# Kernel optimization log

Hardware: AMD Instinct MI355X
Metric: run time of the kernel (lower is better)

## Reference

```python
import jax, jax.numpy as jnp
import numpy as np

N = 4096
IN_F = 512
OUT_F = 64
N_HEADS = 8
ALPHA = 0.2
NEG_INF = -9e15


def setup_inputs() -> dict:
    key = jax.random.key(0)
    k1, k2, k3, k4 = jax.random.split(key, 4)
    h = jax.random.normal(k1, (N, IN_F), dtype=jnp.float32)
    adj = jax.random.randint(k2, (N, N), 0, 2, dtype=jnp.int32)
    W = jax.random.normal(k3, (IN_F, OUT_F * N_HEADS), dtype=jnp.float32) * (1.414 / np.sqrt(IN_F))
    a = jax.random.normal(k4, (2 * OUT_F, 1), dtype=jnp.float32) * 0.1
    return {"h": h, "adj": adj, "W": W, "a": a}


def reference(h, adj, W, a):
    # Wh: [N, H, F]
    Wh = (h @ W).reshape(N, N_HEADS, OUT_F)
    # The all-pairs concat + matmul with a ([2F,1], shared across heads)
    # decomposes exactly: e[i,j,h] = leakyrelu(Wh[i,h]@a[:F] + Wh[j,h]@a[F:])
    a_src = a[:OUT_F, 0]
    a_dst = a[OUT_F:, 0]
    src = jnp.einsum('nhf,f->nh', Wh, a_src)  # [N, H]
    dst = jnp.einsum('nhf,f->nh', Wh, a_dst)  # [N, H]
    e = src[:, None, :] + dst[None, :, :]      # [N, N, H]
    e = jnp.where(e > 0, e, ALPHA * e)         # leaky relu
    e = jnp.where(adj[:, :, None] > 0, e, NEG_INF)
    attention = jax.nn.softmax(e, axis=1)      # softmax over neighbors j
    h_prime = jnp.einsum('ijh,jhf->ihf', attention, Wh)  # [N, H, F]
    out = h_prime.reshape(N, N_HEADS * OUT_F)
    return jax.nn.elu(out)
```

## Files before the change

### kernel.cpp

```cpp
#include <hip/hip_runtime.h>
#include <hip/hip_bf16.h>


typedef unsigned short ushort_t;
typedef __attribute__((ext_vector_type(8))) short bf16x8;
typedef __attribute__((ext_vector_type(4))) float f32x4;

#define LOG2E 1.4426950408889634f

__device__ __forceinline__ ushort_t f2bf(float x) {
    unsigned u = __builtin_bit_cast(unsigned, x);
    u += 0x7FFFu + ((u >> 16) & 1u);
    return (ushort_t)(u >> 16);
}

__global__ __launch_bounds__(256) void transpose_w(const float* __restrict__ W,
                                                   ushort_t* __restrict__ WT) {
    __shared__ ushort_t t[32][33];
    int bx = blockIdx.x & 15, by = blockIdx.x >> 4;
    int tx = threadIdx.x & 31, ty = threadIdx.x >> 5;
#pragma unroll
    for (int i = 0; i < 32; i += 8)
        t[ty + i][tx] = f2bf(W[(by * 32 + ty + i) * 512 + bx * 32 + tx]);
    __syncthreads();
#pragma unroll
    for (int i = 0; i < 32; i += 8)
        WT[(bx * 32 + ty + i) * 512 + by * 32 + tx] = t[tx][ty + i];
}

__global__ __launch_bounds__(256, 4) void gemm_pack(const ushort_t* __restrict__ WT,
                                                    const float* __restrict__ h,
                                                    const float* __restrict__ a,
                                                    ushort_t* __restrict__ WhT,
                                                    float* __restrict__ expA,
                                                    float* __restrict__ expC,
                                                    float* __restrict__ expB,
                                                    float* __restrict__ expD,
                                                    const int* __restrict__ adj,
                                                    unsigned char* __restrict__ pk) {
    __shared__ __align__(16) ushort_t Al[2][64][72];
    __shared__ __align__(16) ushort_t Bl[2][64][72];
    __shared__ float asrc[64], adst[64];
    __shared__ float sred[2][4][64];
    int tid = threadIdx.x;
    if (blockIdx.x >= 512) {
        int pbid = blockIdx.x - 512;
        int wv = tid >> 6, lane = tid & 63;
        int row = pbid * 4 + wv;
        const int* ap = adj + (unsigned)row * 4096 + lane;
        unsigned char* pp = pk + (unsigned)row * 512;
        int g = lane;
        int sv = ((g >> 2) & 1) * 4 + (g & 3);
        int cpar = g >> 3;
#pragma unroll 2
        for (int t = 0; t < 8; t++) {
            unsigned long long m[8];
#pragma unroll
            for (int c8 = 0; c8 < 8; c8++)
                m[c8] = __ballot(ap[(t * 8 + c8) * 64] > 0);
            if (lane < 16) {
                unsigned w = 0;
#pragma unroll
                for (int kq = 0; kq < 4; kq++) {
                    unsigned b = (unsigned)(m[2 * kq + cpar] >> (8 * sv)) & 0xFFu;
                    w |= b << (8 * kq);
                }
                *(unsigned*)(pp + g * 32 + t * 4) = w;
            }
        }
        return;
    }
    int wave = tid >> 6, lane = tid & 63, quad = lane >> 4, nn = lane & 15;
    int mb = blockIdx.x & 7, nb = blockIdx.x >> 3;
    if (tid < 64) {
        asrc[tid] = a[tid] * LOG2E;
        adst[tid] = a[64 + tid] * LOG2E;
    }
    int r = tid >> 2, s0 = tid & 3;
    const ushort_t* Ag = WT + (unsigned)((mb * 64 + r) * 512 + s0 * 8);
    const float* Bg = h + (unsigned)((nb * 64 + r) * 512 + s0 * 8);
    bf16x8 pA0 = *(const bf16x8*)(Ag);
    bf16x8 pA1 = *(const bf16x8*)(Ag + 32);
    float4 pb0 = *(const float4*)(Bg);
    float4 pb1 = *(const float4*)(Bg + 4);
    float4 pb2 = *(const float4*)(Bg + 32);
    float4 pb3 = *(const float4*)(Bg + 36);
    f32x4 acc[4] = {};
#pragma unroll 2
    for (int t = 0; t < 8; t++) {
        int cb = t & 1;
        *(bf16x8*)&Al[cb][r][s0 * 8] = pA0;
        *(bf16x8*)&Al[cb][r][s0 * 8 + 32] = pA1;
        bf16x8 bv;
        bv[0] = (short)f2bf(pb0.x); bv[1] = (short)f2bf(pb0.y);
        bv[2] = (short)f2bf(pb0.z); bv[3] = (short)f2bf(pb0.w);
        bv[4] = (short)f2bf(pb1.x); bv[5] = (short)f2bf(pb1.y);
        bv[6] = (short)f2bf(pb1.z); bv[7] = (short)f2bf(pb1.w);
        *(bf16x8*)&Bl[cb][r][s0 * 8] = bv;
        bv[0] = (short)f2bf(pb2.x); bv[1] = (short)f2bf(pb2.y);
        bv[2] = (short)f2bf(pb2.z); bv[3] = (short)f2bf(pb2.w);
        bv[4] = (short)f2bf(pb3.x); bv[5] = (short)f2bf(pb3.y);
        bv[6] = (short)f2bf(pb3.z); bv[7] = (short)f2bf(pb3.w);
        *(bf16x8*)&Bl[cb][r][s0 * 8 + 32] = bv;
        if (t < 7) {
            int ko = (t + 1) * 64;
            pA0 = *(const bf16x8*)(Ag + ko);
            pA1 = *(const bf16x8*)(Ag + ko + 32);
            pb0 = *(const float4*)(Bg + ko);
            pb1 = *(const float4*)(Bg + ko + 4);
            pb2 = *(const float4*)(Bg + ko + 32);
            pb3 = *(const float4*)(Bg + ko + 36);
        }
        if (t > 0) {
            int pb = cb ^ 1;
            bf16x8 af0 = *(const bf16x8*)&Al[pb][wave * 16 + nn][quad * 8];
            bf16x8 af1 = *(const bf16x8*)&Al[pb][wave * 16 + nn][32 + quad * 8];
#pragma unroll
            for (int nt = 0; nt < 4; nt++) {
                bf16x8 b0 = *(const bf16x8*)&Bl[pb][nt * 16 + nn][quad * 8];
                bf16x8 b1 = *(const bf16x8*)&Bl[pb][nt * 16 + nn][32 + quad * 8];
                acc[nt] = __builtin_amdgcn_mfma_f32_16x16x32_bf16(af0, b0, acc[nt], 0, 0, 0);
                acc[nt] = __builtin_amdgcn_mfma_f32_16x16x32_bf16(af1, b1, acc[nt], 0, 0, 0);
            }
        }
        __syncthreads();
    }
    {
        bf16x8 af0 = *(const bf16x8*)&Al[1][wave * 16 + nn][quad * 8];
        bf16x8 af1 = *(const bf16x8*)&Al[1][wave * 16 + nn][32 + quad * 8];
#pragma unroll
        for (int nt = 0; nt < 4; nt++) {
            bf16x8 b0 = *(const bf16x8*)&Bl[1][nt * 16 + nn][quad * 8];
            bf16x8 b1 = *(const bf16x8*)&Bl[1][nt * 16 + nn][32 + quad * 8];
            acc[nt] = __builtin_amdgcn_mfma_f32_16x16x32_bf16(af0, b0, acc[nt], 0, 0, 0);
            acc[nt] = __builtin_amdgcn_mfma_f32_16x16x32_bf16(af1, b1, acc[nt], 0, 0, 0);
        }
    }
    int row0 = mb * 64 + wave * 16 + quad * 4;
    int col0 = nb * 64 + nn;
    int f0i = wave * 16 + quad * 4;
#pragma unroll
    for (int nt = 0; nt < 4; nt++) {
        float s = 0.f, d = 0.f;
#pragma unroll
        for (int rr = 0; rr < 4; rr++) {
            float v = acc[nt][rr];
            WhT[(unsigned)((row0 + rr) * 4096 + col0 + nt * 16)] = f2bf(v);
            s += v * asrc[f0i + rr];
            d += v * adst[f0i + rr];
        }
        s += __shfl_xor(s, 16); s += __shfl_xor(s, 32);
        d += __shfl_xor(d, 16); d += __shfl_xor(d, 32);
        if (quad == 0) { sred[0][wave][nt * 16 + nn] = s; sred[1][wave][nt * 16 + nn] = d; }
    }
    __syncthreads();
    if (tid < 64) {
        float s = sred[0][0][tid] + sred[0][1][tid] + sred[0][2][tid] + sred[0][3][tid];
        unsigned idx = mb * 4096 + nb * 64 + tid;
        expA[idx] = __builtin_amdgcn_exp2f(s);
        expC[idx] = __builtin_amdgcn_exp2f(0.2f * s);
    } else if (tid < 128) {
        int c = tid - 64;
        float d = sred[1][0][c] + sred[1][1][c] + sred[1][2][c] + sred[1][3][c];
        unsigned idx = mb * 4096 + nb * 64 + c;
        expB[idx] = __builtin_amdgcn_exp2f(d);
        expD[idx] = __builtin_amdgcn_exp2f(0.2f * d);
    }
}

__global__ __launch_bounds__(512, 4) void gat_attn(const unsigned char* __restrict__ pk,
                                                   const ushort_t* __restrict__ WhT,
                                                   const float* __restrict__ expA,
                                                   const float* __restrict__ expC,
                                                   const float* __restrict__ expB,
                                                   const float* __restrict__ expD,
                                                   float* __restrict__ out) {
    __shared__ __align__(16) ushort_t Vb[2][128][136];
    __shared__ float denomp[4][2][32];
    int tid = threadIdx.x;
    int wave = tid >> 6, lane = tid & 63, quad = lane >> 4, nn = lane & 15;
    int hb = blockIdx.x >> 7, ib = blockIdx.x & 127;
    int i0 = ib * 32;
    int whead = wave & 1, jq = wave >> 1;
    int g = jq * 4 + quad;
    int head = hb * 2 + whead;
    float Ai0 = expA[head * 4096 + i0 + nn];
    float Ci0 = expC[head * 4096 + i0 + nn];
    float Ai1 = expA[head * 4096 + i0 + 16 + nn];
    float Ci1 = expC[head * 4096 + i0 + 16 + nn];
    const unsigned char* mpA = pk + (unsigned)(i0 + nn) * 512 + g * 32;
    const unsigned char* mpB = mpA + 16 * 512;
    const float* Bp = expB + (unsigned)head * 4096 + jq * 32 + quad * 8;
    const float* Dp = expD + (unsigned)head * 4096 + jq * 32 + quad * 8;
    int vrow = tid >> 2, vs = tid & 3;
    const ushort_t* Vg = WhT + (unsigned)(hb * 128 + vrow) * 4096 + vs * 8;
    bf16x8 onef;
#pragma unroll
    for (int i = 0; i < 8; i++) onef[i] = (short)0x3F80;
    f32x4 acc[2][4] = {};
    f32x4 accd[2] = {};
    bf16x8 pv[4];
    float4 pBD[4];
    pv[0] = *(const bf16x8*)(Vg);
    pv[1] = *(const bf16x8*)(Vg + 32);
    pv[2] = *(const bf16x8*)(Vg + 64);
    pv[3] = *(const bf16x8*)(Vg + 96);
    pBD[0] = *(const float4*)(Bp);
    pBD[1] = *(const float4*)(Bp + 4);
    pBD[2] = *(const float4*)(Dp);
    pBD[3] = *(const float4*)(Dp + 4);
    unsigned mcA = *(const unsigned*)(mpA);
    unsigned mcB = *(const unsigned*)(mpB);
    unsigned mnA = 0, mnB = 0;
    for (int t = 0; t < 8; t++) {
#pragma unroll
        for (int u = 0; u < 4; u++) {
            int kb = t * 4 + u;
            int cb = kb & 1;
            *(bf16x8*)&Vb[cb][vrow][vs * 8] = pv[0];
            *(bf16x8*)&Vb[cb][vrow][vs * 8 + 32] = pv[1];
            *(bf16x8*)&Vb[cb][vrow][vs * 8 + 64] = pv[2];
            *(bf16x8*)&Vb[cb][vrow][vs * 8 + 96] = pv[3];
            float4 Bv0 = pBD[0], Bv1 = pBD[1], Dv0 = pBD[2], Dv1 = pBD[3];
            bf16x8 af0, af1;
            {
                unsigned w0, w1, w2, w3, w4, w5, w6, w7;
                float w;
                w = fmaxf(Ai0 * Bv0.x, Ci0 * Dv0.x);
                w0 = __builtin_bit_cast(unsigned, w) & 0xFFFF0000u;
                w0 &= (unsigned)__builtin_amdgcn_sbfe(mcA, u * 8 + 0, 1);
                w = fmaxf(Ai0 * Bv0.y, Ci0 * Dv0.y);
                w1 = __builtin_bit_cast(unsigned, w) & 0xFFFF0000u;
                w1 &= (unsigned)__builtin_amdgcn_sbfe(mcA, u * 8 + 1, 1);
                w = fmaxf(Ai0 * Bv0.z, Ci0 * Dv0.z);
                w2 = __builtin_bit_cast(unsigned, w) & 0xFFFF0000u;
                w2 &= (unsigned)__builtin_amdgcn_sbfe(mcA, u * 8 + 2, 1);
                w = fmaxf(Ai0 * Bv0.w, Ci0 * Dv0.w);
                w3 = __builtin_bit_cast(unsigned, w) & 0xFFFF0000u;
                w3 &= (unsigned)__builtin_amdgcn_sbfe(mcA, u * 8 + 3, 1);
                w = fmaxf(Ai0 * Bv1.x, Ci0 * Dv1.x);
                w4 = __builtin_bit_cast(unsigned, w) & 0xFFFF0000u;
                w4 &= (unsigned)__builtin_amdgcn_sbfe(mcA, u * 8 + 4, 1);
                w = fmaxf(Ai0 * Bv1.y, Ci0 * Dv1.y);
                w5 = __builtin_bit_cast(unsigned, w) & 0xFFFF0000u;
                w5 &= (unsigned)__builtin_amdgcn_sbfe(mcA, u * 8 + 5, 1);
                w = fmaxf(Ai0 * Bv1.z, Ci0 * Dv1.z);
                w6 = __builtin_bit_cast(unsigned, w) & 0xFFFF0000u;
                w6 &= (unsigned)__builtin_amdgcn_sbfe(mcA, u * 8 + 6, 1);
                w = fmaxf(Ai0 * Bv1.w, Ci0 * Dv1.w);
                w7 = __builtin_bit_cast(unsigned, w) & 0xFFFF0000u;
                w7 &= (unsigned)__builtin_amdgcn_sbfe(mcA, u * 8 + 7, 1);
                uint4 pq;
                pq.x = __builtin_amdgcn_perm(w1, w0, 0x07060302u);
                pq.y = __builtin_amdgcn_perm(w3, w2, 0x07060302u);
                pq.z = __builtin_amdgcn_perm(w5, w4, 0x07060302u);
                pq.w = __builtin_amdgcn_perm(w7, w6, 0x07060302u);
                af0 = __builtin_bit_cast(bf16x8, pq);
                w = fmaxf(Ai1 * Bv0.x, Ci1 * Dv0.x);
                w0 = __builtin_bit_cast(unsigned, w) & 0xFFFF0000u;
                w0 &= (unsigned)__builtin_amdgcn_sbfe(mcB, u * 8 + 0, 1);
                w = fmaxf(Ai1 * Bv0.y, Ci1 * Dv0.y);
                w1 = __builtin_bit_cast(unsigned, w) & 0xFFFF0000u;
                w1 &= (unsigned)__builtin_amdgcn_sbfe(mcB, u * 8 + 1, 1);
                w = fmaxf(Ai1 * Bv0.z, Ci1 * Dv0.z);
                w2 = __builtin_bit_cast(unsigned, w) & 0xFFFF0000u;
                w2 &= (unsigned)__builtin_amdgcn_sbfe(mcB, u * 8 + 2, 1);
                w = fmaxf(Ai1 * Bv0.w, Ci1 * Dv0.w);
                w3 = __builtin_bit_cast(unsigned, w) & 0xFFFF0000u;
                w3 &= (unsigned)__builtin_amdgcn_sbfe(mcB, u * 8 + 3, 1);
                w = fmaxf(Ai1 * Bv1.x, Ci1 * Dv1.x);
                w4 = __builtin_bit_cast(unsigned, w) & 0xFFFF0000u;
                w4 &= (unsigned)__builtin_amdgcn_sbfe(mcB, u * 8 + 4, 1);
                w = fmaxf(Ai1 * Bv1.y, Ci1 * Dv1.y);
                w5 = __builtin_bit_cast(unsigned, w) & 0xFFFF0000u;
                w5 &= (unsigned)__builtin_amdgcn_sbfe(mcB, u * 8 + 5, 1);
                w = fmaxf(Ai1 * Bv1.z, Ci1 * Dv1.z);
                w6 = __builtin_bit_cast(unsigned, w) & 0xFFFF0000u;
                w6 &= (unsigned)__builtin_amdgcn_sbfe(mcB, u * 8 + 6, 1);
                w = fmaxf(Ai1 * Bv1.w, Ci1 * Dv1.w);
                w7 = __builtin_bit_cast(unsigned, w) & 0xFFFF0000u;
                w7 &= (unsigned)__builtin_amdgcn_sbfe(mcB, u * 8 + 7, 1);
                pq.x = __builtin_amdgcn_perm(w1, w0, 0x07060302u);
                pq.y = __builtin_amdgcn_perm(w3, w2, 0x07060302u);
                pq.z = __builtin_amdgcn_perm(w5, w4, 0x07060302u);
                pq.w = __builtin_amdgcn_perm(w7, w6, 0x07060302u);
                af1 = __builtin_bit_cast(bf16x8, pq);
            }
            if (u == 3) { mcA = mnA; mcB = mnB; }
            __syncthreads();
            __builtin_amdgcn_sched_barrier(0);
            if (kb < 31) {
                const ushort_t* vp = Vg + (kb + 1) * 128;
                pv[0] = *(const bf16x8*)(vp);
                pv[1] = *(const bf16x8*)(vp + 32);
                pv[2] = *(const bf16x8*)(vp + 64);
                pv[3] = *(const bf16x8*)(vp + 96);
                pBD[0] = *(const float4*)(Bp + (kb + 1) * 128);
                pBD[1] = *(const float4*)(Bp + (kb + 1) * 128 + 4);
                pBD[2] = *(const float4*)(Dp + (kb + 1) * 128);
                pBD[3] = *(const float4*)(Dp + (kb + 1) * 128 + 4);
            }
            if (u == 0 && t < 7) {
                mnA = *(const unsigned*)(mpA + (t + 1) * 4);
                mnB = *(const unsigned*)(mpB + (t + 1) * 4);
            }
#pragma unroll
            for (int nt = 0; nt < 4; nt++) {
                bf16x8 bv = *(const bf16x8*)&Vb[cb][whead * 64 + nt * 16 + nn][jq * 32 + quad * 8];
                acc[0][nt] = __builtin_amdgcn_mfma_f32_16x16x32_bf16(af0, bv, acc[0][nt], 0, 0, 0);
                acc[1][nt] = __builtin_amdgcn_mfma_f32_16x16x32_bf16(af1, bv, acc[1][nt], 0, 0, 0);
            }
            accd[0] = __builtin_amdgcn_mfma_f32_16x16x32_bf16(af0, onef, accd[0], 0, 0, 0);
            accd[1] = __builtin_amdgcn_mfma_f32_16x16x32_bf16(af1, onef, accd[1], 0, 0, 0);
        }
    }
    __syncthreads();
    if (nn == 0) {
#pragma unroll
        for (int s = 0; s < 2; s++)
#pragma unroll
            for (int rr = 0; rr < 4; rr++)
                denomp[jq][whead][s * 16 + quad * 4 + rr] = accd[s][rr];
    }
    float (*cmb)[3][64][32] = reinterpret_cast<float (*)[3][64][32]>(&Vb[0][0][0]);
    if (jq > 0) {
#pragma unroll
        for (int s = 0; s < 2; s++)
#pragma unroll
            for (int nt = 0; nt < 4; nt++)
                *(f32x4*)&cmb[whead][jq - 1][lane][s * 16 + nt * 4] = acc[s][nt];
    }
    __syncthreads();
    if (jq == 0) {
#pragma unroll
        for (int s = 0; s < 2; s++) {
#pragma unroll
            for (int nt = 0; nt < 4; nt++) {
                f32x4 o = acc[s][nt]
                        + *(const f32x4*)&cmb[whead][0][lane][s * 16 + nt * 4]
                        + *(const f32x4*)&cmb[whead][1][lane][s * 16 + nt * 4]
                        + *(const f32x4*)&cmb[whead][2][lane][s * 16 + nt * 4];
#pragma unroll
                for (int rr = 0; rr < 4; rr++) {
                    int il = s * 16 + quad * 4 + rr;
                    float dnm = fmaxf(denomp[0][whead][il] + denomp[1][whead][il]
                                    + denomp[2][whead][il] + denomp[3][whead][il], 1e-30f);
                    float v = o[rr] / dnm;
                    v = v > 0.f ? v : __expf(v) - 1.f;
                    out[(unsigned)(i0 + il) * 512 + hb * 128 + whead * 64 + nt * 16 + nn] = v;
                }
            }
        }
    }
}

extern "C" void kernel_launch(void* const* d_in, const int* in_sizes, int n_in,
                              void* d_out, int out_size, void* d_ws, size_t ws_size,
                              hipStream_t stream) {
    const float* h   = (const float*)d_in[0];
    const int*   adj = (const int*)d_in[1];
    const float* W   = (const float*)d_in[2];
    const float* a   = (const float*)d_in[3];

    char* ws = (char*)d_ws;
    ushort_t* WhT = (ushort_t*)ws;
    ushort_t* WT  = (ushort_t*)(ws + (4u << 20));
    float* expA = (float*)(ws + (4u << 20) + (512u << 10));
    float* expC = expA + 8 * 4096;
    float* expB = expC + 8 * 4096;
    float* expD = expB + 8 * 4096;
    unsigned char* pkm = (unsigned char*)(ws + (5u << 20));

    transpose_w<<<256, 256, 0, stream>>>(W, WT);
    gemm_pack<<<1536, 256, 0, stream>>>(WT, h, a, WhT, expA, expC, expB, expD,
                                        adj, pkm);
    gat_attn<<<512, 512, 0, stream>>>(pkm, WhT, expA, expC, expB, expD,
                                      (float*)d_out);
}
```

Before: 169.7 us.

## Load V fragments directly from global into registers, drop LDS staging and barriers

The attention loop no longer stages the WhT tile through double-buffered shared memory. Each lane now loads its MFMA B-operand fragments straight from global memory into ping-pong register sets, which removes the per-iteration LDS stores, LDS reads and __syncthreads. The MFMA block is also wrapped in s_setprio to favour matrix issue. In exchange, each V element is fetched from global or L2 by several waves, since the two heads share rows and the reads are strided, and register pressure rises with two fragment sets.

```diff
diff --git a/kernel.cpp b/kernel.cpp
--- a/kernel.cpp
+++ b/kernel.cpp
@@ -168,6 +168,79 @@
     }
 }
 
+__device__ __forceinline__ bf16x8 gen_frag(float Ai, float Ci,
+                                           float4 Bv0, float4 Bv1,
+                                           float4 Dv0, float4 Dv1,
+                                           unsigned mc, int u) {
+    unsigned w0, w1, w2, w3, w4, w5, w6, w7;
+    float w;
+    w = fmaxf(Ai * Bv0.x, Ci * Dv0.x);
+    w0 = __builtin_bit_cast(unsigned, w) & 0xFFFF0000u;
+    w0 &= (unsigned)__builtin_amdgcn_sbfe(mc, u * 8 + 0, 1);
+    w = fmaxf(Ai * Bv0.y, Ci * Dv0.y);
+    w1 = __builtin_bit_cast(unsigned, w) & 0xFFFF0000u;
+    w1 &= (unsigned)__builtin_amdgcn_sbfe(mc, u * 8 + 1, 1);
+    w = fmaxf(Ai * Bv0.z, Ci * Dv0.z);
+    w2 = __builtin_bit_cast(unsigned, w) & 0xFFFF0000u;
+    w2 &= (unsigned)__builtin_amdgcn_sbfe(mc, u * 8 + 2, 1);
+    w = fmaxf(Ai * Bv0.w, Ci * Dv0.w);
+    w3 = __builtin_bit_cast(unsigned, w) & 0xFFFF0000u;
+    w3 &= (unsigned)__builtin_amdgcn_sbfe(mc, u * 8 + 3, 1);
+    w = fmaxf(Ai * Bv1.x, Ci * Dv1.x);
+    w4 = __builtin_bit_cast(unsigned, w) & 0xFFFF0000u;
+    w4 &= (unsigned)__builtin_amdgcn_sbfe(mc, u * 8 + 4, 1);
+    w = fmaxf(Ai * Bv1.y, Ci * Dv1.y);
+    w5 = __builtin_bit_cast(unsigned, w) & 0xFFFF0000u;
+    w5 &= (unsigned)__builtin_amdgcn_sbfe(mc, u * 8 + 5, 1);
+    w = fmaxf(Ai * Bv1.z, Ci * Dv1.z);
+    w6 = __builtin_bit_cast(unsigned, w) & 0xFFFF0000u;
+    w6 &= (unsigned)__builtin_amdgcn_sbfe(mc, u * 8 + 6, 1);
+    w = fmaxf(Ai * Bv1.w, Ci * Dv1.w);
+    w7 = __builtin_bit_cast(unsigned, w) & 0xFFFF0000u;
+    w7 &= (unsigned)__builtin_amdgcn_sbfe(mc, u * 8 + 7, 1);
+    uint4 pq;
+    pq.x = __builtin_amdgcn_perm(w1, w0, 0x07060302u);
+    pq.y = __builtin_amdgcn_perm(w3, w2, 0x07060302u);
+    pq.z = __builtin_amdgcn_perm(w5, w4, 0x07060302u);
+    pq.w = __builtin_amdgcn_perm(w7, w6, 0x07060302u);
+    return __builtin_bit_cast(bf16x8, pq);
+}
+
+#define ATT_BODY(UU, PC, PN)                                                          \
+    {                                                                                 \
+        const int kb = t * 4 + UU;                                                    \
+        bf16x8 af0 = gen_frag(Ai0, Ci0, pBD[0], pBD[1], pBD[2], pBD[3], mcA, UU);     \
+        bf16x8 af1 = gen_frag(Ai1, Ci1, pBD[0], pBD[1], pBD[2], pBD[3], mcB, UU);     \
+        if (UU == 3) { mcA = mnA; mcB = mnB; }                                        \
+        if (kb < 31) {                                                               \
+            const ushort_t* vp = Vg + (kb + 1) * 128;                                 \
+            PN[0] = *(const bf16x8*)(vp);                                             \
+            PN[1] = *(const bf16x8*)(vp + 65536);                                     \
+            PN[2] = *(const bf16x8*)(vp + 131072);                                    \
+            PN[3] = *(const bf16x8*)(vp + 196608);                                    \
+            pBD[0] = *(const float4*)(Bp + (kb + 1) * 128);                           \
+            pBD[1] = *(const float4*)(Bp + (kb + 1) * 128 + 4);                       \
+            pBD[2] = *(const float4*)(Dp + (kb + 1) * 128);                           \
+            pBD[3] = *(const float4*)(Dp + (kb + 1) * 128 + 4);                       \
+        }                                                                             \
+        if (UU == 0 && t < 7) {                                                       \
+            mnA = *(const unsigned*)(mpA + (t + 1) * 4);                              \
+            mnB = *(const unsigned*)(mpB + (t + 1) * 4);                              \
+        }                                                                             \
+        __builtin_amdgcn_s_setprio(1);                                                \
+        acc[0][0] = __builtin_amdgcn_mfma_f32_16x16x32_bf16(af0, PC[0], acc[0][0], 0, 0, 0); \
+        acc[1][0] = __builtin_amdgcn_mfma_f32_16x16x32_bf16(af1, PC[0], acc[1][0], 0, 0, 0); \
+        acc[0][1] = __builtin_amdgcn_mfma_f32_16x16x32_bf16(af0, PC[1], acc[0][1], 0, 0, 0); \
+        acc[1][1] = __builtin_amdgcn_mfma_f32_16x16x32_bf16(af1, PC[1], acc[1][1], 0, 0, 0); \
+        acc[0][2] = __builtin_amdgcn_mfma_f32_16x16x32_bf16(af0, PC[2], acc[0][2], 0, 0, 0); \
+        acc[1][2] = __builtin_amdgcn_mfma_f32_16x16x32_bf16(af1, PC[2], acc[1][2], 0, 0, 0); \
+        acc[0][3] = __builtin_amdgcn_mfma_f32_16x16x32_bf16(af0, PC[3], acc[0][3], 0, 0, 0); \
+        acc[1][3] = __builtin_amdgcn_mfma_f32_16x16x32_bf16(af1, PC[3], acc[1][3], 0, 0, 0); \
+        accd[0] = __builtin_amdgcn_mfma_f32_16x16x32_bf16(af0, onef, accd[0], 0, 0, 0);      \
+        accd[1] = __builtin_amdgcn_mfma_f32_16x16x32_bf16(af1, onef, accd[1], 0, 0, 0);      \
+        __builtin_amdgcn_s_setprio(0);                                                \
+    }
+
 __global__ __launch_bounds__(512, 4) void gat_attn(const unsigned char* __restrict__ pk,
                                                    const ushort_t* __restrict__ WhT,
                                                    const float* __restrict__ expA,
@@ -175,7 +248,7 @@
                                                    const float* __restrict__ expB,
                                                    const float* __restrict__ expD,
                                                    float* __restrict__ out) {
-    __shared__ __align__(16) ushort_t Vb[2][128][136];
+    __shared__ __align__(16) float cmb[2][3][64][32];
     __shared__ float denomp[4][2][32];
     int tid = threadIdx.x;
     int wave = tid >> 6, lane = tid & 63, quad = lane >> 4, nn = lane & 15;
@@ -192,19 +265,19 @@
     const unsigned char* mpB = mpA + 16 * 512;
     const float* Bp = expB + (unsigned)head * 4096 + jq * 32 + quad * 8;
     const float* Dp = expD + (unsigned)head * 4096 + jq * 32 + quad * 8;
-    int vrow = tid >> 2, vs = tid & 3;
-    const ushort_t* Vg = WhT + (unsigned)(hb * 128 + vrow) * 4096 + vs * 8;
+    const ushort_t* Vg = WhT + (unsigned)(hb * 128 + whead * 64 + nn) * 4096
+                             + jq * 32 + quad * 8;
     bf16x8 onef;
 #pragma unroll
     for (int i = 0; i < 8; i++) onef[i] = (short)0x3F80;
     f32x4 acc[2][4] = {};
     f32x4 accd[2] = {};
-    bf16x8 pv[4];
+    bf16x8 pva[4], pvb[4];
     float4 pBD[4];
-    pv[0] = *(const bf16x8*)(Vg);
-    pv[1] = *(const bf16x8*)(Vg + 32);
-    pv[2] = *(const bf16x8*)(Vg + 64);
-    pv[3] = *(const bf16x8*)(Vg + 96);
+    pva[0] = *(const bf16x8*)(Vg);
+    pva[1] = *(const bf16x8*)(Vg + 65536);
+    pva[2] = *(const bf16x8*)(Vg + 131072);
+    pva[3] = *(const bf16x8*)(Vg + 196608);
     pBD[0] = *(const float4*)(Bp);
     pBD[1] = *(const float4*)(Bp + 4);
     pBD[2] = *(const float4*)(Dp);
@@ -213,108 +286,11 @@
     unsigned mcB = *(const unsigned*)(mpB);
     unsigned mnA = 0, mnB = 0;
     for (int t = 0; t < 8; t++) {
-#pragma unroll
-        for (int u = 0; u < 4; u++) {
-            int kb = t * 4 + u;
-            int cb = kb & 1;
-            *(bf16x8*)&Vb[cb][vrow][vs * 8] = pv[0];
-            *(bf16x8*)&Vb[cb][vrow][vs * 8 + 32] = pv[1];
-            *(bf16x8*)&Vb[cb][vrow][vs * 8 + 64] = pv[2];
-            *(bf16x8*)&Vb[cb][vrow][vs * 8 + 96] = pv[3];
-            float4 Bv0 = pBD[0], Bv1 = pBD[1], Dv0 = pBD[2], Dv1 = pBD[3];
-            bf16x8 af0, af1;
-            {
-                unsigned w0, w1, w2, w3, w4, w5, w6, w7;
-                float w;
-                w = fmaxf(Ai0 * Bv0.x, Ci0 * Dv0.x);
-                w0 = __builtin_bit_cast(unsigned, w) & 0xFFFF0000u;
-                w0 &= (unsigned)__builtin_amdgcn_sbfe(mcA, u * 8 + 0, 1);
-                w = fmaxf(Ai0 * Bv0.y, Ci0 * Dv0.y);
-                w1 = __builtin_bit_cast(unsigned, w) & 0xFFFF0000u;
-                w1 &= (unsigned)__builtin_amdgcn_sbfe(mcA, u * 8 + 1, 1);
-                w = fmaxf(Ai0 * Bv0.z, Ci0 * Dv0.z);
-                w2 = __builtin_bit_cast(unsigned, w) & 0xFFFF0000u;
-                w2 &= (unsigned)__builtin_amdgcn_sbfe(mcA, u * 8 + 2, 1);
-                w = fmaxf(Ai0 * Bv0.w, Ci0 * Dv0.w);
-                w3 = __builtin_bit_cast(unsigned, w) & 0xFFFF0000u;
-                w3 &= (unsigned)__builtin_amdgcn_sbfe(mcA, u * 8 + 3, 1);
-                w = fmaxf(Ai0 * Bv1.x, Ci0 * Dv1.x);
-                w4 = __builtin_bit_cast(unsigned, w) & 0xFFFF0000u;
-                w4 &= (unsigned)__builtin_amdgcn_sbfe(mcA, u * 8 + 4, 1);
-                w = fmaxf(Ai0 * Bv1.y, Ci0 * Dv1.y);
-                w5 = __builtin_bit_cast(unsigned, w) & 0xFFFF0000u;
-                w5 &= (unsigned)__builtin_amdgcn_sbfe(mcA, u * 8 + 5, 1);
-                w = fmaxf(Ai0 * Bv1.z, Ci0 * Dv1.z);
-                w6 = __builtin_bit_cast(unsigned, w) & 0xFFFF0000u;
-                w6 &= (unsigned)__builtin_amdgcn_sbfe(mcA, u * 8 + 6, 1);
-                w = fmaxf(Ai0 * Bv1.w, Ci0 * Dv1.w);
-                w7 = __builtin_bit_cast(unsigned, w) & 0xFFFF0000u;
-                w7 &= (unsigned)__builtin_amdgcn_sbfe(mcA, u * 8 + 7, 1);
-                uint4 pq;
-                pq.x = __builtin_amdgcn_perm(w1, w0, 0x07060302u);
-                pq.y = __builtin_amdgcn_perm(w3, w2, 0x07060302u);
-                pq.z = __builtin_amdgcn_perm(w5, w4, 0x07060302u);
-                pq.w = __builtin_amdgcn_perm(w7, w6, 0x07060302u);
-                af0 = __builtin_bit_cast(bf16x8, pq);
-                w = fmaxf(Ai1 * Bv0.x, Ci1 * Dv0.x);
-                w0 = __builtin_bit_cast(unsigned, w) & 0xFFFF0000u;
-                w0 &= (unsigned)__builtin_amdgcn_sbfe(mcB, u * 8 + 0, 1);
-                w = fmaxf(Ai1 * Bv0.y, Ci1 * Dv0.y);
-                w1 = __builtin_bit_cast(unsigned, w) & 0xFFFF0000u;
-                w1 &= (unsigned)__builtin_amdgcn_sbfe(mcB, u * 8 + 1, 1);
-                w = fmaxf(Ai1 * Bv0.z, Ci1 * Dv0.z);
-                w2 = __builtin_bit_cast(unsigned, w) & 0xFFFF0000u;
-                w2 &= (unsigned)__builtin_amdgcn_sbfe(mcB, u * 8 + 2, 1);
-                w = fmaxf(Ai1 * Bv0.w, Ci1 * Dv0.w);
-                w3 = __builtin_bit_cast(unsigned, w) & 0xFFFF0000u;
-                w3 &= (unsigned)__builtin_amdgcn_sbfe(mcB, u * 8 + 3, 1);
-                w = fmaxf(Ai1 * Bv1.x, Ci1 * Dv1.x);
-                w4 = __builtin_bit_cast(unsigned, w) & 0xFFFF0000u;
-                w4 &= (unsigned)__builtin_amdgcn_sbfe(mcB, u * 8 + 4, 1);
-                w = fmaxf(Ai1 * Bv1.y, Ci1 * Dv1.y);
-                w5 = __builtin_bit_cast(unsigned, w) & 0xFFFF0000u;
-                w5 &= (unsigned)__builtin_amdgcn_sbfe(mcB, u * 8 + 5, 1);
-                w = fmaxf(Ai1 * Bv1.z, Ci1 * Dv1.z);
-                w6 = __builtin_bit_cast(unsigned, w) & 0xFFFF0000u;
-                w6 &= (unsigned)__builtin_amdgcn_sbfe(mcB, u * 8 + 6, 1);
-                w = fmaxf(Ai1 * Bv1.w, Ci1 * Dv1.w);
-                w7 = __builtin_bit_cast(unsigned, w) & 0xFFFF0000u;
-                w7 &= (unsigned)__builtin_amdgcn_sbfe(mcB, u * 8 + 7, 1);
-                pq.x = __builtin_amdgcn_perm(w1, w0, 0x07060302u);
-                pq.y = __builtin_amdgcn_perm(w3, w2, 0x07060302u);
-                pq.z = __builtin_amdgcn_perm(w5, w4, 0x07060302u);
-                pq.w = __builtin_amdgcn_perm(w7, w6, 0x07060302u);
-                af1 = __builtin_bit_cast(bf16x8, pq);
-            }
-            if (u == 3) { mcA = mnA; mcB = mnB; }
-            __syncthreads();
-            __builtin_amdgcn_sched_barrier(0);
-            if (kb < 31) {
-                const ushort_t* vp = Vg + (kb + 1) * 128;
-                pv[0] = *(const bf16x8*)(vp);
-                pv[1] = *(const bf16x8*)(vp + 32);
-                pv[2] = *(const bf16x8*)(vp + 64);
-                pv[3] = *(const bf16x8*)(vp + 96);
-                pBD[0] = *(const float4*)(Bp + (kb + 1) * 128);
-                pBD[1] = *(const float4*)(Bp + (kb + 1) * 128 + 4);
-                pBD[2] = *(const float4*)(Dp + (kb + 1) * 128);
-                pBD[3] = *(const float4*)(Dp + (kb + 1) * 128 + 4);
-            }
-            if (u == 0 && t < 7) {
-                mnA = *(const unsigned*)(mpA + (t + 1) * 4);
-                mnB = *(const unsigned*)(mpB + (t + 1) * 4);
-            }
-#pragma unroll
-            for (int nt = 0; nt < 4; nt++) {
-                bf16x8 bv = *(const bf16x8*)&Vb[cb][whead * 64 + nt * 16 + nn][jq * 32 + quad * 8];
-                acc[0][nt] = __builtin_amdgcn_mfma_f32_16x16x32_bf16(af0, bv, acc[0][nt], 0, 0, 0);
-                acc[1][nt] = __builtin_amdgcn_mfma_f32_16x16x32_bf16(af1, bv, acc[1][nt], 0, 0, 0);
-            }
-            accd[0] = __builtin_amdgcn_mfma_f32_16x16x32_bf16(af0, onef, accd[0], 0, 0, 0);
-            accd[1] = __builtin_amdgcn_mfma_f32_16x16x32_bf16(af1, onef, accd[1], 0, 0, 0);
-        }
-    }
-    __syncthreads();
+        ATT_BODY(0, pva, pvb)
+        ATT_BODY(1, pvb, pva)
+        ATT_BODY(2, pva, pvb)
+        ATT_BODY(3, pvb, pva)
+    }
     if (nn == 0) {
 #pragma unroll
         for (int s = 0; s < 2; s++)
@@ -322,7 +298,6 @@
             for (int rr = 0; rr < 4; rr++)
                 denomp[jq][whead][s * 16 + quad * 4 + rr] = accd[s][rr];
     }
-    float (*cmb)[3][64][32] = reinterpret_cast<float (*)[3][64][32]>(&Vb[0][0][0]);
     if (jq > 0) {
 #pragma unroll
         for (int s = 0; s < 2; s++)
```

New measurement: 229.2 us. +35.1%, slower.

## Single-buffer V tile in LDS to raise occupancy, split epilogue reduction

Applied to the files above, without the earlier changes.

Replaces the double-buffered V tile in shared memory with a single buffer, adding a second barrier per step so writes and reads don't overlap. The epilogue reduction is split into two halves so the smaller LDS region suffices, and the V store mapping is remapped per wave. Launch bounds raise the minimum blocks per SM from 4 to 8 to exploit lower LDS use. This trades extra synchronisation and register pressure limits for more resident blocks and latency hiding.

```diff
diff --git a/kernel.cpp b/kernel.cpp
--- a/kernel.cpp
+++ b/kernel.cpp
@@ -168,14 +168,14 @@
     }
 }
 
-__global__ __launch_bounds__(512, 4) void gat_attn(const unsigned char* __restrict__ pk,
+__global__ __launch_bounds__(512, 8) void gat_attn(const unsigned char* __restrict__ pk,
                                                    const ushort_t* __restrict__ WhT,
                                                    const float* __restrict__ expA,
                                                    const float* __restrict__ expC,
                                                    const float* __restrict__ expB,
                                                    const float* __restrict__ expD,
                                                    float* __restrict__ out) {
-    __shared__ __align__(16) ushort_t Vb[2][128][136];
+    __shared__ __align__(16) ushort_t Vb[128][136];
     __shared__ float denomp[4][2][32];
     int tid = threadIdx.x;
     int wave = tid >> 6, lane = tid & 63, quad = lane >> 4, nn = lane & 15;
@@ -192,7 +192,8 @@
     const unsigned char* mpB = mpA + 16 * 512;
     const float* Bp = expB + (unsigned)head * 4096 + jq * 32 + quad * 8;
     const float* Dp = expD + (unsigned)head * 4096 + jq * 32 + quad * 8;
-    int vrow = tid >> 2, vs = tid & 3;
+    int vrow = (wave << 4) | (tid & 15);
+    int vs = (tid >> 4) & 3;
     const ushort_t* Vg = WhT + (unsigned)(hb * 128 + vrow) * 4096 + vs * 8;
     bf16x8 onef;
 #pragma unroll
@@ -216,11 +217,6 @@
 #pragma unroll
         for (int u = 0; u < 4; u++) {
             int kb = t * 4 + u;
-            int cb = kb & 1;
-            *(bf16x8*)&Vb[cb][vrow][vs * 8] = pv[0];
-            *(bf16x8*)&Vb[cb][vrow][vs * 8 + 32] = pv[1];
-            *(bf16x8*)&Vb[cb][vrow][vs * 8 + 64] = pv[2];
-            *(bf16x8*)&Vb[cb][vrow][vs * 8 + 96] = pv[3];
             float4 Bv0 = pBD[0], Bv1 = pBD[1], Dv0 = pBD[2], Dv1 = pBD[3];
             bf16x8 af0, af1;
             {
@@ -287,8 +283,13 @@
                 af1 = __builtin_bit_cast(bf16x8, pq);
             }
             if (u == 3) { mcA = mnA; mcB = mnB; }
+            accd[0] = __builtin_amdgcn_mfma_f32_16x16x32_bf16(af0, onef, accd[0], 0, 0, 0);
+            accd[1] = __builtin_amdgcn_mfma_f32_16x16x32_bf16(af1, onef, accd[1], 0, 0, 0);
             __syncthreads();
-            __builtin_amdgcn_sched_barrier(0);
+            *(bf16x8*)&Vb[vrow][vs * 8] = pv[0];
+            *(bf16x8*)&Vb[vrow][vs * 8 + 32] = pv[1];
+            *(bf16x8*)&Vb[vrow][vs * 8 + 64] = pv[2];
+            *(bf16x8*)&Vb[vrow][vs * 8 + 96] = pv[3];
             if (kb < 31) {
                 const ushort_t* vp = Vg + (kb + 1) * 128;
                 pv[0] = *(const bf16x8*)(vp);
@@ -304,14 +305,14 @@
                 mnA = *(const unsigned*)(mpA + (t + 1) * 4);
                 mnB = *(const unsigned*)(mpB + (t + 1) * 4);
             }
+            __syncthreads();
+            __builtin_amdgcn_sched_barrier(0);
 #pragma unroll
             for (int nt = 0; nt < 4; nt++) {
-                bf16x8 bv = *(const bf16x8*)&Vb[cb][whead * 64 + nt * 16 + nn][jq * 32 + quad * 8];
+                bf16x8 bv = *(const bf16x8*)&Vb[whead * 64 + nt * 16 + nn][jq * 32 + quad * 8];
                 acc[0][nt] = __builtin_amdgcn_mfma_f32_16x16x32_bf16(af0, bv, acc[0][nt], 0, 0, 0);
                 acc[1][nt] = __builtin_amdgcn_mfma_f32_16x16x32_bf16(af1, bv, acc[1][nt], 0, 0, 0);
             }
-            accd[0] = __builtin_amdgcn_mfma_f32_16x16x32_bf16(af0, onef, accd[0], 0, 0, 0);
-            accd[1] = __builtin_amdgcn_mfma_f32_16x16x32_bf16(af1, onef, accd[1], 0, 0, 0);
         }
     }
     __syncthreads();
@@ -322,24 +323,22 @@
             for (int rr = 0; rr < 4; rr++)
                 denomp[jq][whead][s * 16 + quad * 4 + rr] = accd[s][rr];
     }
-    float (*cmb)[3][64][32] = reinterpret_cast<float (*)[3][64][32]>(&Vb[0][0][0]);
-    if (jq > 0) {
-#pragma unroll
-        for (int s = 0; s < 2; s++)
+    float (*cmb)[3][64][16] = reinterpret_cast<float (*)[3][64][16]>(&Vb[0][0]);
+#pragma unroll
+    for (int s = 0; s < 2; s++) {
+        if (jq > 0) {
 #pragma unroll
             for (int nt = 0; nt < 4; nt++)
-                *(f32x4*)&cmb[whead][jq - 1][lane][s * 16 + nt * 4] = acc[s][nt];
-    }
-    __syncthreads();
-    if (jq == 0) {
-#pragma unroll
-        for (int s = 0; s < 2; s++) {
+                *(f32x4*)&cmb[whead][jq - 1][lane][nt * 4] = acc[s][nt];
+        }
+        __syncthreads();
+        if (jq == 0) {
 #pragma unroll
             for (int nt = 0; nt < 4; nt++) {
                 f32x4 o = acc[s][nt]
-                        + *(const f32x4*)&cmb[whead][0][lane][s * 16 + nt * 4]
-                        + *(const f32x4*)&cmb[whead][1][lane][s * 16 + nt * 4]
-                        + *(const f32x4*)&cmb[whead][2][lane][s * 16 + nt * 4];
+                        + *(const f32x4*)&cmb[whead][0][lane][nt * 4]
+                        + *(const f32x4*)&cmb[whead][1][lane][nt * 4]
+                        + *(const f32x4*)&cmb[whead][2][lane][nt * 4];
 #pragma unroll
                 for (int rr = 0; rr < 4; rr++) {
                     int il = s * 16 + quad * 4 + rr;
@@ -351,6 +350,7 @@
                 }
             }
         }
+        if (s == 0) __syncthreads();
     }
 }
 
```

Measured after the change: 571.2 us. 237% more time.

## Stage V tiles with direct global-to-LDS loads and an XOR-swizzled layout

Applied to the files above, without the earlier changes.

The V tile of the attention kernel used to be loaded into registers and then written to padded LDS. It is now copied straight from global memory into LDS with global_load_lds 16-byte transfers, double-buffered one step ahead. Row padding is dropped and replaced by an XOR swizzle on both the write and read addresses to avoid bank conflicts. This removes the register staging and the ds_write instructions, which should lower VGPR pressure and instruction count. The risks are correct wait-count handling for the asynchronous LDS writes and a subtler addressing scheme.

```diff
diff --git a/kernel.cpp b/kernel.cpp
--- a/kernel.cpp
+++ b/kernel.cpp
@@ -12,6 +12,12 @@
     unsigned u = __builtin_bit_cast(unsigned, x);
     u += 0x7FFFu + ((u >> 16) & 1u);
     return (ushort_t)(u >> 16);
+}
+
+__device__ __forceinline__ void gload16(const void* g, void* l) {
+    __builtin_amdgcn_global_load_lds(
+        (const __attribute__((address_space(1))) unsigned int*)g,
+        (__attribute__((address_space(3))) unsigned int*)l, 16, 0, 0);
 }
 
 __global__ __launch_bounds__(256) void transpose_w(const float* __restrict__ W,
@@ -175,7 +181,7 @@
                                                    const float* __restrict__ expB,
                                                    const float* __restrict__ expD,
                                                    float* __restrict__ out) {
-    __shared__ __align__(16) ushort_t Vb[2][128][136];
+    __shared__ __align__(16) ushort_t Vb[2][128][128];
     __shared__ float denomp[4][2][32];
     int tid = threadIdx.x;
     int wave = tid >> 6, lane = tid & 63, quad = lane >> 4, nn = lane & 15;
@@ -192,19 +198,28 @@
     const unsigned char* mpB = mpA + 16 * 512;
     const float* Bp = expB + (unsigned)head * 4096 + jq * 32 + quad * 8;
     const float* Dp = expD + (unsigned)head * 4096 + jq * 32 + quad * 8;
-    int vrow = tid >> 2, vs = tid & 3;
-    const ushort_t* Vg = WhT + (unsigned)(hb * 128 + vrow) * 4096 + vs * 8;
+    int hh = lane >> 4, lg = lane & 15;
+    const ushort_t* stg0 = WhT + (unsigned)(hb * 128 + wave * 16 + 0 + hh) * 4096
+                               + ((lg ^ (hh << 2) ^ 0) * 8);
+    const ushort_t* stg1 = WhT + (unsigned)(hb * 128 + wave * 16 + 4 + hh) * 4096
+                               + ((lg ^ (hh << 2) ^ 1) * 8);
+    const ushort_t* stg2 = WhT + (unsigned)(hb * 128 + wave * 16 + 8 + hh) * 4096
+                               + ((lg ^ (hh << 2) ^ 2) * 8);
+    const ushort_t* stg3 = WhT + (unsigned)(hb * 128 + wave * 16 + 12 + hh) * 4096
+                               + ((lg ^ (hh << 2) ^ 3) * 8);
+    char* lwb = (char*)&Vb[0][0][0] + wave * 4096;
+    int rcol = (jq * 64 + quad * 16) ^ ((((nn & 3) << 2) | ((nn >> 2) & 3)) << 4);
+    const char* vrb = (const char*)&Vb[0][0][0] + (whead * 64 + nn) * 256 + rcol;
     bf16x8 onef;
 #pragma unroll
     for (int i = 0; i < 8; i++) onef[i] = (short)0x3F80;
     f32x4 acc[2][4] = {};
     f32x4 accd[2] = {};
-    bf16x8 pv[4];
     float4 pBD[4];
-    pv[0] = *(const bf16x8*)(Vg);
-    pv[1] = *(const bf16x8*)(Vg + 32);
-    pv[2] = *(const bf16x8*)(Vg + 64);
-    pv[3] = *(const bf16x8*)(Vg + 96);
+    gload16(stg0, lwb);
+    gload16(stg1, lwb + 1024);
+    gload16(stg2, lwb + 2048);
+    gload16(stg3, lwb + 3072);
     pBD[0] = *(const float4*)(Bp);
     pBD[1] = *(const float4*)(Bp + 4);
     pBD[2] = *(const float4*)(Dp);
@@ -216,11 +231,7 @@
 #pragma unroll
         for (int u = 0; u < 4; u++) {
             int kb = t * 4 + u;
-            int cb = kb & 1;
-            *(bf16x8*)&Vb[cb][vrow][vs * 8] = pv[0];
-            *(bf16x8*)&Vb[cb][vrow][vs * 8 + 32] = pv[1];
-            *(bf16x8*)&Vb[cb][vrow][vs * 8 + 64] = pv[2];
-            *(bf16x8*)&Vb[cb][vrow][vs * 8 + 96] = pv[3];
+            int cb = u & 1;
             float4 Bv0 = pBD[0], Bv1 = pBD[1], Dv0 = pBD[2], Dv1 = pBD[3];
             bf16x8 af0, af1;
             {
@@ -290,11 +301,12 @@
             __syncthreads();
             __builtin_amdgcn_sched_barrier(0);
             if (kb < 31) {
-                const ushort_t* vp = Vg + (kb + 1) * 128;
-                pv[0] = *(const bf16x8*)(vp);
-                pv[1] = *(const bf16x8*)(vp + 32);
-                pv[2] = *(const bf16x8*)(vp + 64);
-                pv[3] = *(const bf16x8*)(vp + 96);
+                char* lb = (char*)&Vb[0][0][0] + wave * 4096 + ((cb ^ 1) << 15);
+                gload16(stg0 + 128, lb);
+                gload16(stg1 + 128, lb + 1024);
+                gload16(stg2 + 128, lb + 2048);
+                gload16(stg3 + 128, lb + 3072);
+                stg0 += 128; stg1 += 128; stg2 += 128; stg3 += 128;
                 pBD[0] = *(const float4*)(Bp + (kb + 1) * 128);
                 pBD[1] = *(const float4*)(Bp + (kb + 1) * 128 + 4);
                 pBD[2] = *(const float4*)(Dp + (kb + 1) * 128);
@@ -306,7 +318,7 @@
             }
 #pragma unroll
             for (int nt = 0; nt < 4; nt++) {
-                bf16x8 bv = *(const bf16x8*)&Vb[cb][whead * 64 + nt * 16 + nn][jq * 32 + quad * 8];
+                bf16x8 bv = *(const bf16x8*)(vrb + (cb << 15) + nt * 4096);
                 acc[0][nt] = __builtin_amdgcn_mfma_f32_16x16x32_bf16(af0, bv, acc[0][nt], 0, 0, 0);
                 acc[1][nt] = __builtin_amdgcn_mfma_f32_16x16x32_bf16(af1, bv, acc[1][nt], 0, 0, 0);
             }
```

After: 175.8 us. +3.6%, slower.
